# Kernel optimization log

Hardware: AMD Instinct MI355X
Metric: run time of the kernel (lower is better)

## Reference

```python
import jax, jax.numpy as jnp
import numpy as np

N_NODES = 50000
N_EDGES = 640000
N_REL = 8
IN_DIM = 128
HID_DIM = 128
OUT_DIM = 64


def setup_inputs() -> dict:
    key = jax.random.key(0)
    ks = jax.random.split(key, 8)
    features = jax.random.normal(ks[0], (N_NODES, IN_DIM), dtype=jnp.float32)
    src = jax.random.randint(ks[1], (N_EDGES,), 0, N_NODES, dtype=jnp.int32)
    dst = jax.random.randint(ks[2], (N_EDGES,), 0, N_NODES, dtype=jnp.int32)
    edge_types = jax.random.randint(ks[3], (N_EDGES,), 0, N_REL, dtype=jnp.int32)
    s1 = 1.0 / np.sqrt(IN_DIM)
    s2 = 1.0 / np.sqrt(HID_DIM)
    W1 = jax.random.normal(ks[4], (N_REL, IN_DIM, HID_DIM), dtype=jnp.float32) * s1
    W1_self = jax.random.normal(ks[5], (IN_DIM, HID_DIM), dtype=jnp.float32) * s1
    b1 = jnp.zeros((HID_DIM,), dtype=jnp.float32)
    W2 = jax.random.normal(ks[6], (N_REL, HID_DIM, OUT_DIM), dtype=jnp.float32) * s2
    W2_self = jax.random.normal(ks[7], (HID_DIM, OUT_DIM), dtype=jnp.float32) * s2
    b2 = jnp.zeros((OUT_DIM,), dtype=jnp.float32)
    return {"features": features, "src": src, "dst": dst, "edge_types": edge_types,
            "W1": W1, "W1_self": W1_self, "b1": b1,
            "W2": W2, "W2_self": W2_self, "b2": b2}


def _rel_graph_conv(h, src, dst, edge_types, W, W_self, b):
    # Precompute relation-specific transforms for all nodes: [R, N, Dout]
    rel = jnp.einsum('nd,rdo->rno', h, W)
    # Gather per-edge message W[etype(e)] @ h[src(e)]: [E, Dout]
    msg = rel[edge_types, src]
    # Scatter-sum to destination nodes
    agg = jax.ops.segment_sum(msg, dst, num_segments=h.shape[0])
    # Self-loop + bias (DGL RelGraphConv defaults: self_loop=True, bias=True)
    return agg + h @ W_self + b


def reference(features, src, dst, edge_types, W1, W1_self, b1, W2, W2_self, b2):
    h = jax.nn.relu(_rel_graph_conv(features, src, dst, edge_types, W1, W1_self, b1))
    logits = _rel_graph_conv(h, src, dst, edge_types, W2, W2_self, b2)
    return logits
```

## Files before the change

kernel.cpp:

```cpp
#include <hip/hip_runtime.h>
#include <hip/hip_bf16.h>
#include <stdint.h>

#define NN 50000
#define NE 640000
#define NR 8
#define NK (NR * NN)
#define NPB 391

typedef short bf16x8 __attribute__((ext_vector_type(8)));
typedef float f32x4  __attribute__((ext_vector_type(4)));

__device__ __forceinline__ unsigned short f2bf(float f) {
    union { float f; unsigned u; } v; v.f = f;
    unsigned r = v.u + 0x7FFF + ((v.u >> 16) & 1);
    return (unsigned short)(r >> 16);
}

__global__ __launch_bounds__(256) void prep_hist_kernel(
        const float* __restrict__ X,
        const float* __restrict__ W1, const float* __restrict__ W1s,
        const float* __restrict__ W2, const float* __restrict__ W2s,
        const int* __restrict__ dst, const int* __restrict__ et,
        unsigned short* __restrict__ Xbf,
        unsigned char* __restrict__ Xq8, float* __restrict__ Xsc,
        unsigned short* __restrict__ W1T, unsigned short* __restrict__ W2T,
        int* __restrict__ counts) {
    const int gid = blockIdx.x * 256 + threadIdx.x;
    const int gsz = gridDim.x * 256;

    for (int e = gid; e < NE; e += gsz)
        atomicAdd(&counts[et[e] * NN + dst[e]], 1);

    for (int i = gid; i < NN * 16; i += gsz) {
        const float4* pp = (const float4*)X + (size_t)i * 2;
        float4 a = pp[0], b = pp[1];
        float f[8] = {a.x, a.y, a.z, a.w, b.x, b.y, b.z, b.w};
        uint4 o;
        o.x = (unsigned)f2bf(f[0]) | ((unsigned)f2bf(f[1]) << 16);
        o.y = (unsigned)f2bf(f[2]) | ((unsigned)f2bf(f[3]) << 16);
        o.z = (unsigned)f2bf(f[4]) | ((unsigned)f2bf(f[5]) << 16);
        o.w = (unsigned)f2bf(f[6]) | ((unsigned)f2bf(f[7]) << 16);
        ((uint4*)Xbf)[i] = o;

        float mx = 0.f;
        #pragma unroll
        for (int j = 0; j < 8; j++) mx = fmaxf(mx, fabsf(f[j]));
        #pragma unroll
        for (int m = 1; m < 16; m <<= 1) mx = fmaxf(mx, __shfl_xor(mx, m, 64));
        float inv = (mx > 0.f) ? 127.f / mx : 0.f;
        int q[8];
        #pragma unroll
        for (int j = 0; j < 8; j++) q[j] = __float2int_rn(f[j] * inv);
        uint2 qp;
        qp.x = (q[0] & 0xFF) | ((q[1] & 0xFF) << 8) | ((q[2] & 0xFF) << 16) | ((unsigned)(q[3] & 0xFF) << 24);
        qp.y = (q[4] & 0xFF) | ((q[5] & 0xFF) << 8) | ((q[6] & 0xFF) << 16) | ((unsigned)(q[7] & 0xFF) << 24);
        ((uint2*)Xq8)[i] = qp;
        if ((i & 15) == 0) Xsc[i >> 4] = mx * (1.f / 127.f);
    }

    for (int i = gid; i < 9 * 128 * 128; i += gsz) {
        int k = i & 127, c = i >> 7;
        int r = c >> 7, o = c & 127;
        float v = (r < 8) ? W1[((size_t)r * 128 + k) * 128 + o]
                          : W1s[(size_t)k * 128 + o];
        W1T[i] = f2bf(v);
    }

    for (int i = gid; i < 9 * 64 * 128; i += gsz) {
        int k = i & 127, c = i >> 7;
        int r = c >> 6, o = c & 63;
        float v = (r < 8) ? W2[((size_t)r * 128 + k) * 64 + o]
                          : W2s[(size_t)k * 64 + o];
        W2T[i] = f2bf(v);
    }
}

__global__ __launch_bounds__(1024) void blocksum_kernel(const int* __restrict__ counts,
                                                        int* __restrict__ bsum, int n) {
    __shared__ int ws[16];
    int i = blockIdx.x * 1024 + threadIdx.x;
    int v = (i < n) ? counts[i] : 0;
    #pragma unroll
    for (int d = 32; d > 0; d >>= 1) v += __shfl_down(v, d, 64);
    int wid = threadIdx.x >> 6, lane = threadIdx.x & 63;
    if (lane == 0) ws[wid] = v;
    __syncthreads();
    if (threadIdx.x < 16) {
        int s = ws[threadIdx.x];
        #pragma unroll
        for (int d = 8; d > 0; d >>= 1) s += __shfl_down(s, d, 16);
        if (threadIdx.x == 0) bsum[blockIdx.x] = s;
    }
}

__global__ __launch_bounds__(1024) void scanlocal2_kernel(const int* __restrict__ counts,
                                                          const int* __restrict__ bsum,
                                                          int* __restrict__ offsets,
                                                          int* __restrict__ cursor, int n) {
    __shared__ int ws[16];
    __shared__ int wbase[16];
    __shared__ int base_sh;
    const int t = threadIdx.x, b = blockIdx.x;
    const int i = b * 1024 + t;
    const int lane = t & 63, wid = t >> 6;

    int v = (i < n) ? counts[i] : 0;
    int incl = v;
    #pragma unroll
    for (int d = 1; d < 64; d <<= 1) {
        int nv = __shfl_up(incl, d, 64);
        if (lane >= d) incl += nv;
    }
    if (lane == 63) ws[wid] = incl;
    __syncthreads();
    if (t < 16) {
        int s = ws[t], si = s;
        #pragma unroll
        for (int d = 1; d < 16; d <<= 1) {
            int nv = __shfl_up(si, d, 16);
            if (t >= d) si += nv;
        }
        wbase[t] = si - s;
    }
    __syncthreads();
    int local_excl = wbase[wid] + incl - v;

    if (wid == 0) {
        int acc = 0;
        for (int j = lane; j < b; j += 64) acc += bsum[j];
        #pragma unroll
        for (int d = 32; d > 0; d >>= 1) acc += __shfl_down(acc, d, 64);
        if (lane == 0) base_sh = acc;
    }
    __syncthreads();

    if (i < n) {
        int excl = base_sh + local_excl;
        offsets[i] = excl;
        cursor[i]  = excl;
    }
    if (b == 0 && t == 0) offsets[NK] = NE;
}

__global__ void fill2_kernel(const int* __restrict__ src, const int* __restrict__ dst,
                             const int* __restrict__ et, int* __restrict__ cursor,
                             int* __restrict__ esrc) {
    int e = blockIdx.x * 256 + threadIdx.x;
    if (e < NE) {
        int pos = atomicAdd(&cursor[et[e] * NN + dst[e]], 1);
        esrc[pos] = src[e];
    }
}

template<int NOUT, bool RELU, bool OUTBF16, bool GQ8>
__global__ __launch_bounds__(256) void fused_layer(
        const unsigned short* __restrict__ A,
        const unsigned char*  __restrict__ Aq,
        const float* __restrict__ Asc,
        const unsigned short* __restrict__ WT,
        const float* __restrict__ bias,
        const int* __restrict__ off2,
        const int* __restrict__ esrc,
        void* __restrict__ outp,
        int M) {
    constexpr int CW = NOUT / 4;
    constexpr int NJ = CW / 16;
    __shared__ unsigned short Asw[64 * 128];

    const int t = threadIdx.x;
    const int n0 = blockIdx.x * 64;
    const int bm = (M - n0 < 64) ? (M - n0) : 64;
    const int lane = t & 63;
    const int w = t >> 6;
    const int r15 = lane & 15;
    const int q = lane >> 4;

    const int key = t >> 2;
    const int sub = t & 3;
    const int kk = n0 + key;
    const bool kv = (kk < M);

    f32x4 acc[4][NJ] = {};

    auto do_mfma = [&](int rr) {
        #pragma unroll
        for (int ks = 0; ks < 4; ks++) {
            int c = (ks * 4 + q) ^ r15;
            bf16x8 af[4];
            #pragma unroll
            for (int i = 0; i < 4; i++)
                af[i] = *(const bf16x8*)((const char*)Asw + (i * 16 + r15) * 256 + (c << 4));
            #pragma unroll
            for (int j = 0; j < NJ; j++) {
                bf16x8 bf = *(const bf16x8*)(WT +
                    ((size_t)(rr * NOUT + w * CW + j * 16 + r15) << 7) + ks * 32 + q * 8);
                #pragma unroll
                for (int i = 0; i < 4; i++)
                    acc[i][j] = __builtin_amdgcn_mfma_f32_16x16x32_bf16(af[i], bf, acc[i][j], 0, 0, 0);
            }
        }
    };

    int e0 = kv ? off2[kk] : 0;
    int e1 = kv ? off2[kk + 1] : 0;

    #pragma unroll
    for (int kc = 0; kc < 4; kc++) {
        int g = t + kc * 256;
        int row = g >> 4, c = g & 15;
        uint4 v = make_uint4(0, 0, 0, 0);
        if (row < bm) v = *(const uint4*)(A + ((size_t)(n0 + row) << 7) + c * 8);
        *(uint4*)((char*)Asw + row * 256 + ((c ^ (row & 15)) << 4)) = v;
    }
    __syncthreads();
    do_mfma(8);

    for (int r = 0; r < 8; r++) {
        int e0n = 0, e1n = 0;
        if (r < 7 && kv) {
            e0n = off2[(r + 1) * NN + kk];
            e1n = off2[(r + 1) * NN + kk + 1];
        }

        float a[32];
        #pragma unroll
        for (int i = 0; i < 32; i++) a[i] = 0.f;
        for (int e = e0; e < e1; ++e) {
            int s = esrc[e];
            if (GQ8) {
                float sc = Asc[s];
                const uint4* rp = (const uint4*)(Aq + ((size_t)s << 7) + sub * 32);
                uint4 q0 = rp[0], q1 = rp[1];
                unsigned uu[8] = {q0.x, q0.y, q0.z, q0.w, q1.x, q1.y, q1.z, q1.w};
                #pragma unroll
                for (int d = 0; d < 8; ++d) {
                    unsigned x = uu[d];
                    a[d * 4 + 0] = fmaf((float)((int)(x << 24) >> 24), sc, a[d * 4 + 0]);
                    a[d * 4 + 1] = fmaf((float)((int)(x << 16) >> 24), sc, a[d * 4 + 1]);
                    a[d * 4 + 2] = fmaf((float)((int)(x <<  8) >> 24), sc, a[d * 4 + 2]);
                    a[d * 4 + 3] = fmaf((float)((int)x >> 24),         sc, a[d * 4 + 3]);
                }
            } else {
                const uint4* rp = (const uint4*)((const unsigned*)A + ((size_t)s << 6) + sub * 16);
                #pragma unroll
                for (int u4 = 0; u4 < 4; ++u4) {
                    uint4 v = rp[u4];
                    unsigned uu[4] = {v.x, v.y, v.z, v.w};
                    #pragma unroll
                    for (int j = 0; j < 4; ++j) {
                        a[u4 * 8 + j * 2 + 0] += __uint_as_float(uu[j] << 16);
                        a[u4 * 8 + j * 2 + 1] += __uint_as_float(uu[j] & 0xffff0000u);
                    }
                }
            }
        }
        __syncthreads();

        #pragma unroll
        for (int c4 = 0; c4 < 4; ++c4) {
            uint4 pv;
            pv.x = (unsigned)f2bf(a[c4 * 8 + 0]) | ((unsigned)f2bf(a[c4 * 8 + 1]) << 16);
            pv.y = (unsigned)f2bf(a[c4 * 8 + 2]) | ((unsigned)f2bf(a[c4 * 8 + 3]) << 16);
            pv.z = (unsigned)f2bf(a[c4 * 8 + 4]) | ((unsigned)f2bf(a[c4 * 8 + 5]) << 16);
            pv.w = (unsigned)f2bf(a[c4 * 8 + 6]) | ((unsigned)f2bf(a[c4 * 8 + 7]) << 16);
            int c = sub * 4 + c4;
            *(uint4*)((char*)Asw + key * 256 + ((c ^ (key & 15)) << 4)) = pv;
        }
        __syncthreads();

        do_mfma(r);
        e0 = e0n; e1 = e1n;
    }

    #pragma unroll
    for (int j = 0; j < NJ; j++) {
        int col = w * CW + j * 16 + r15;
        float bv = bias[col];
        #pragma unroll
        for (int i = 0; i < 4; i++) {
            #pragma unroll
            for (int reg = 0; reg < 4; reg++) {
                int m = n0 + i * 16 + q * 4 + reg;
                if (m < M) {
                    float v = acc[i][j][reg] + bv;
                    if (RELU) v = fmaxf(v, 0.f);
                    if (OUTBF16)
                        ((unsigned short*)outp)[(size_t)m * NOUT + col] = f2bf(v);
                    else
                        ((float*)outp)[(size_t)m * NOUT + col] = v;
                }
            }
        }
    }
}

extern "C" void kernel_launch(void* const* d_in, const int* in_sizes, int n_in,
                              void* d_out, int out_size, void* d_ws, size_t ws_size,
                              hipStream_t stream) {
    const float* X   = (const float*)d_in[0];
    const int*   src = (const int*)d_in[1];
    const int*   dst = (const int*)d_in[2];
    const int*   et  = (const int*)d_in[3];
    const float* W1  = (const float*)d_in[4];
    const float* W1s = (const float*)d_in[5];
    const float* b1  = (const float*)d_in[6];
    const float* W2  = (const float*)d_in[7];
    const float* W2s = (const float*)d_in[8];
    const float* b2  = (const float*)d_in[9];
    float* out = (float*)d_out;

    char* p = (char*)d_ws;
    unsigned short* Xbf = (unsigned short*)p; p += (size_t)NN * 128 * 2;
    unsigned short* hbf = (unsigned short*)p; p += (size_t)NN * 128 * 2;
    unsigned short* W1T = (unsigned short*)p; p += (size_t)9 * 128 * 128 * 2;
    unsigned short* W2T = (unsigned short*)p; p += (size_t)9 * 64 * 128 * 2;
    int* counts2 = (int*)p; p += (size_t)NK * 4;
    int* off2    = (int*)p; p += (size_t)(NK + 4) * 4;
    int* cursor2 = (int*)p; p += (size_t)NK * 4;
    int* esrc    = (int*)p; p += (size_t)NE * 4;
    int* bsum    = (int*)p; p += 512 * 4;
    int* bbase   = (int*)p; p += 512 * 4;
    unsigned char* Xq8 = (unsigned char*)p; p += (size_t)NN * 128;
    float* Xsc = (float*)p; p += (size_t)NN * 4;

    hipMemsetAsync(counts2, 0, (size_t)NK * sizeof(int), stream);
    prep_hist_kernel<<<2048, 256, 0, stream>>>(X, W1, W1s, W2, W2s, dst, et,
                                               Xbf, Xq8, Xsc, W1T, W2T, counts2);
    blocksum_kernel<<<NPB, 1024, 0, stream>>>(counts2, bsum, NK);
    scanlocal2_kernel<<<NPB, 1024, 0, stream>>>(counts2, bsum, off2, cursor2, NK);
    fill2_kernel<<<(NE + 255) / 256, 256, 0, stream>>>(src, dst, et, cursor2, esrc);

    const int nblk = (NN + 63) / 64;

    fused_layer<128, true, true, true><<<nblk, 256, 0, stream>>>(
        Xbf, Xq8, Xsc, W1T, b1, off2, esrc, hbf, NN);
    fused_layer<64, false, false, false><<<nblk, 256, 0, stream>>>(
        hbf, nullptr, nullptr, W2T, b2, off2, esrc, out, NN);
}
```

Before: 285.3 us.

## Quantize hidden layer to int8 with per-32-column scales for layer-2 gather

Switches the int8 quantization of features from one scale per row to four scales per row, one per 32-column quarter, matching the sub-lane split used in the gather. Layer 1 now also writes an int8 copy of the hidden activations plus per-quarter scales in its epilogue, so layer 2 can gather int8 rows instead of bf16 rows. This halves the bytes read per edge in the second layer's neighbor aggregation. The cost is extra shuffles and byte stores in the layer-1 epilogue, more workspace, and additional quantization error in layer 2.

```diff
diff --git a/kernel.cpp b/kernel.cpp
--- a/kernel.cpp
+++ b/kernel.cpp
@@ -47,7 +47,7 @@
         #pragma unroll
         for (int j = 0; j < 8; j++) mx = fmaxf(mx, fabsf(f[j]));
         #pragma unroll
-        for (int m = 1; m < 16; m <<= 1) mx = fmaxf(mx, __shfl_xor(mx, m, 64));
+        for (int m = 1; m < 4; m <<= 1) mx = fmaxf(mx, __shfl_xor(mx, m, 64));
         float inv = (mx > 0.f) ? 127.f / mx : 0.f;
         int q[8];
         #pragma unroll
@@ -56,7 +56,7 @@
         qp.x = (q[0] & 0xFF) | ((q[1] & 0xFF) << 8) | ((q[2] & 0xFF) << 16) | ((unsigned)(q[3] & 0xFF) << 24);
         qp.y = (q[4] & 0xFF) | ((q[5] & 0xFF) << 8) | ((q[6] & 0xFF) << 16) | ((unsigned)(q[7] & 0xFF) << 24);
         ((uint2*)Xq8)[i] = qp;
-        if ((i & 15) == 0) Xsc[i >> 4] = mx * (1.f / 127.f);
+        if ((i & 3) == 0) Xsc[(i >> 4) * 4 + ((i >> 2) & 3)] = mx * (1.f / 127.f);
     }
 
     for (int i = gid; i < 9 * 128 * 128; i += gsz) {
@@ -163,6 +163,8 @@
         const int* __restrict__ off2,
         const int* __restrict__ esrc,
         void* __restrict__ outp,
+        unsigned char* __restrict__ outq,
+        float* __restrict__ outsc,
         int M) {
     constexpr int CW = NOUT / 4;
     constexpr int NJ = CW / 16;
@@ -229,7 +231,7 @@
         for (int e = e0; e < e1; ++e) {
             int s = esrc[e];
             if (GQ8) {
-                float sc = Asc[s];
+                float sc = Asc[s * 4 + sub];
                 const uint4* rp = (const uint4*)(Aq + ((size_t)s << 7) + sub * 32);
                 uint4 q0 = rp[0], q1 = rp[1];
                 unsigned uu[8] = {q0.x, q0.y, q0.z, q0.w, q1.x, q1.y, q1.z, q1.w};
@@ -273,22 +275,53 @@
         e0 = e0n; e1 = e1n;
     }
 
-    #pragma unroll
-    for (int j = 0; j < NJ; j++) {
-        int col = w * CW + j * 16 + r15;
-        float bv = bias[col];
+    if (OUTBF16) {
         #pragma unroll
         for (int i = 0; i < 4; i++) {
             #pragma unroll
             for (int reg = 0; reg < 4; reg++) {
                 int m = n0 + i * 16 + q * 4 + reg;
+                float v[NJ];
+                #pragma unroll
+                for (int j = 0; j < NJ; j++) {
+                    float x = acc[i][j][reg] + bias[w * CW + j * 16 + r15];
+                    if (RELU) x = fmaxf(x, 0.f);
+                    v[j] = x;
+                }
+                float mx = 0.f;
+                #pragma unroll
+                for (int j = 0; j < NJ; j++) mx = fmaxf(mx, fabsf(v[j]));
+                #pragma unroll
+                for (int msk = 1; msk < 16; msk <<= 1)
+                    mx = fmaxf(mx, __shfl_xor(mx, msk, 64));
+                float inv = (mx > 0.f) ? 127.f / mx : 0.f;
                 if (m < M) {
-                    float v = acc[i][j][reg] + bv;
-                    if (RELU) v = fmaxf(v, 0.f);
-                    if (OUTBF16)
-                        ((unsigned short*)outp)[(size_t)m * NOUT + col] = f2bf(v);
-                    else
+                    #pragma unroll
+                    for (int j = 0; j < NJ; j++) {
+                        int col = w * CW + j * 16 + r15;
+                        ((unsigned short*)outp)[(size_t)m * NOUT + col] = f2bf(v[j]);
+                        int qv = __float2int_rn(v[j] * inv);
+                        outq[(size_t)m * 128 + col] = (unsigned char)(qv & 0xFF);
+                    }
+                    if (r15 == 0) outsc[m * 4 + w] = mx * (1.f / 127.f);
+                }
+            }
+        }
+    } else {
+        #pragma unroll
+        for (int j = 0; j < NJ; j++) {
+            int col = w * CW + j * 16 + r15;
+            float bv = bias[col];
+            #pragma unroll
+            for (int i = 0; i < 4; i++) {
+                #pragma unroll
+                for (int reg = 0; reg < 4; reg++) {
+                    int m = n0 + i * 16 + q * 4 + reg;
+                    if (m < M) {
+                        float v = acc[i][j][reg] + bv;
+                        if (RELU) v = fmaxf(v, 0.f);
                         ((float*)outp)[(size_t)m * NOUT + col] = v;
+                    }
                 }
             }
         }
@@ -322,7 +355,9 @@
     int* bsum    = (int*)p; p += 512 * 4;
     int* bbase   = (int*)p; p += 512 * 4;
     unsigned char* Xq8 = (unsigned char*)p; p += (size_t)NN * 128;
-    float* Xsc = (float*)p; p += (size_t)NN * 4;
+    float* Xsc = (float*)p; p += (size_t)NN * 4 * 4;
+    unsigned char* hq8 = (unsigned char*)p; p += (size_t)NN * 128;
+    float* Hsc = (float*)p; p += (size_t)NN * 4 * 4;
 
     hipMemsetAsync(counts2, 0, (size_t)NK * sizeof(int), stream);
     prep_hist_kernel<<<2048, 256, 0, stream>>>(X, W1, W1s, W2, W2s, dst, et,
@@ -334,7 +369,7 @@
     const int nblk = (NN + 63) / 64;
 
     fused_layer<128, true, true, true><<<nblk, 256, 0, stream>>>(
-        Xbf, Xq8, Xsc, W1T, b1, off2, esrc, hbf, NN);
-    fused_layer<64, false, false, false><<<nblk, 256, 0, stream>>>(
-        hbf, nullptr, nullptr, W2T, b2, off2, esrc, out, NN);
-}
+        Xbf, Xq8, Xsc, W1T, b1, off2, esrc, hbf, hq8, Hsc, NN);
+    fused_layer<64, false, false, true><<<nblk, 256, 0, stream>>>(
+        hbf, hq8, Hsc, W2T, b2, off2, esrc, out, nullptr, nullptr, NN);
+}
```

Result: slower. 318.2 us (+11.6%).
